# Performance work log

Measured on AMD Instinct MI355X. Metric: run time of the kernel, lower is better.

Reference implementation:

```python
import jax, jax.numpy as jnp
import numpy as np

TANH_CLIP = 10.0
TEMP = 1.0


def setup_inputs() -> dict:
    key = jax.random.key(0)
    ks = jax.random.split(key, 8)
    B, N, E, H, SC = 1024, 1000, 128, 8, 256
    dk = E // H
    context = jax.random.normal(ks[0], (B, 1, E), dtype=jnp.float32)
    step_context = jax.random.normal(ks[1], (B, 1, SC), dtype=jnp.float32)
    # scale weights so tanh/softmax stay in a sane numeric range
    W_step = jax.random.normal(ks[2], (E, SC), dtype=jnp.float32) * 0.05
    glimpse_K = jax.random.normal(ks[3], (H, B, 1, N, dk), dtype=jnp.float32)
    glimpse_V = jax.random.normal(ks[4], (H, B, 1, N, dk), dtype=jnp.float32)
    logit_K = jax.random.normal(ks[5], (B, 1, N, E), dtype=jnp.float32)
    W_out = jax.random.normal(ks[6], (E, E), dtype=jnp.float32) * 0.05
    mask = jax.random.randint(ks[7], (B, 1, N), 0, 2).astype(bool)
    mask = mask.at[:, :, 0].set(False)  # guarantee at least one feasible node
    return {"context": context, "step_context": step_context, "W_step": W_step,
            "glimpse_K": glimpse_K, "glimpse_V": glimpse_V, "logit_K": logit_K,
            "W_out": W_out, "mask": mask}


def reference(context, step_context, W_step, glimpse_K, glimpse_V, logit_K, W_out, mask):
    B, S, E = context.shape          # S = num_steps = 1
    H = glimpse_K.shape[0]
    dk = E // H
    neg_inf = jnp.float32(-jnp.inf)
    # query = context_node_projected + project_step_context(step_context)
    query = context + jnp.einsum('bsc,ec->bse', step_context, W_step)  # [B,S,E]
    # split heads: glimpse_Q -> [H,B,S,dk] (the singleton q-dim of the torch code is folded)
    Q = query.reshape(B, S, H, dk).transpose(2, 0, 1, 3)
    # compatibility [H,B,S,N]
    compat = jnp.einsum('hbsk,hbsnk->hbsn', Q, glimpse_K) / jnp.sqrt(jnp.float32(dk))
    compat = jnp.where(mask[None], neg_inf, compat)       # mask_inner
    attn = jax.nn.softmax(compat, axis=-1)
    heads = jnp.einsum('hbsn,hbsnk->hbsk', attn, glimpse_V)  # [H,B,S,dk]
    glimpse = heads.transpose(1, 2, 0, 3).reshape(B, S, E)   # concat heads
    glimpse = jnp.einsum('bse,oe->bso', glimpse, W_out)      # project_out
    # logits against logit_K  [B,S,N]
    logits = jnp.einsum('bse,bsne->bsn', glimpse, logit_K) / jnp.sqrt(jnp.float32(E))
    logits = jnp.tanh(logits) * jnp.float32(TANH_CLIP)       # tanh clipping
    logits = jnp.where(mask, neg_inf, logits)                # mask_logits
    log_p = jax.nn.log_softmax(logits / jnp.float32(TEMP), axis=-1)
    return log_p
```

## Files before the change

### kernel.cpp

```cpp
#include <hip/hip_runtime.h>
#include <hip/hip_bf16.h>
#include <math.h>

#define NB  1024
#define NN  1000
#define NE  128
#define NH  8
#define NDK 16
#define NSC 256

typedef __attribute__((ext_vector_type(4))) float f32x4;

__device__ __forceinline__ f32x4 ld4(const float* p) {
    return *reinterpret_cast<const f32x4*>(p);
}

__global__ __launch_bounds__(128)
void query_kernel(const float* __restrict__ ctx, const float* __restrict__ stepc,
                  const float* __restrict__ Wstep, float* __restrict__ q_ws)
{
    const int b = blockIdx.x, t = threadIdx.x;
    __shared__ float sc[NSC];
    sc[t] = stepc[b * NSC + t];
    sc[t + 128] = stepc[b * NSC + t + 128];
    __syncthreads();
    float acc = ctx[b * NE + t];
    const float4* w4 = reinterpret_cast<const float4*>(Wstep + (size_t)t * NSC);
    #pragma unroll 8
    for (int c4 = 0; c4 < NSC / 4; ++c4) {
        float4 w = w4[c4];
        acc += sc[4*c4] * w.x + sc[4*c4+1] * w.y + sc[4*c4+2] * w.z + sc[4*c4+3] * w.w;
    }
    q_ws[b * NE + t] = acc;
}

__global__ __launch_bounds__(512, 4)
void fused_kernel(const float* __restrict__ q_ws,
                  const float* __restrict__ gK, const float* __restrict__ gV,
                  const float* __restrict__ lK, const float* __restrict__ Wout,
                  const unsigned char* __restrict__ mask,
                  __hip_bfloat16* __restrict__ out)
{
    const int b = blockIdx.x;
    const int t = threadIdx.x;
    const int w = t >> 6, lane = t & 63;
    const int qq  = lane & 3;
    const int rsl = lane >> 2;

    __shared__ float wmax[2][8], wsum[2][8];
    __shared__ __align__(16) float wred[2][8][16];
    __shared__ __align__(16) float g[NE];
    __shared__ __align__(16) float gout[NE];
    __shared__ float red[8];
    __shared__ float Mv, LSv;

    const unsigned int* mw = reinterpret_cast<const unsigned int*>(mask);
    const bool m_i32 = (__ballot(mw[lane] <= 1u) == ~0ull);
    const int* mask_i = reinterpret_cast<const int*>(mask);

    unsigned mbits = 0;
    #pragma unroll
    for (int i = 0; i < 8; ++i) {
        const int n = w * 16 + i * 128 + rsl;
        const bool dead = (n >= NN);
        const int nn = dead ? 0 : n;
        int mk = m_i32 ? (mask_i[(size_t)b * NN + nn] != 0)
                       : (mask[(size_t)b * NN + nn] != 0);
        mbits |= (unsigned)(mk | (dead ? 1 : 0)) << i;
    }

    #pragma unroll 1
    for (int h = 0; h < NH; ++h) {
        const int pb = h & 1;
        const f32x4 qv = ld4(q_ws + (size_t)b * NE + h * NDK + qq * 4);
        const float* Kb = gK + (size_t)(h * NB + b) * NN * NDK;
        const float* Vb = gV + (size_t)(h * NB + b) * NN * NDK;

        f32x4 vreg[8];
        float sc[8];
        #pragma unroll
        for (int i = 0; i < 8; ++i) {
            const int n = w * 16 + i * 128 + rsl;
            const int nn = ((mbits >> i) & 1u) ? 0 : n;
            const size_t off = (size_t)nn * NDK + qq * 4;
            f32x4 kv = ld4(Kb + off);
            vreg[i] = ld4(Vb + off);
            sc[i] = kv.x*qv.x + kv.y*qv.y + kv.z*qv.z + kv.w*qv.w;
        }
        #pragma unroll
        for (int i = 0; i < 8; ++i) {
            float p = sc[i];
            p += __shfl_xor(p, 1);
            p += __shfl_xor(p, 2);
            sc[i] = ((mbits >> i) & 1u) ? -INFINITY : p * 0.25f;
        }

        float m = sc[0];
        #pragma unroll
        for (int i = 1; i < 8; ++i) m = fmaxf(m, sc[i]);
        #pragma unroll
        for (int off = 32; off > 0; off >>= 1) m = fmaxf(m, __shfl_xor(m, off));
        if (lane == 0) wmax[pb][w] = m;
        __syncthreads();
        float M = wmax[pb][0];
        #pragma unroll
        for (int i = 1; i < 8; ++i) M = fmaxf(M, wmax[pb][i]);

        f32x4 acc = {0.f, 0.f, 0.f, 0.f};
        float ls = 0.f;
        #pragma unroll
        for (int i = 0; i < 8; ++i) {
            const float e = expf(sc[i] - M);
            ls += e;
            acc.x += e * vreg[i].x; acc.y += e * vreg[i].y;
            acc.z += e * vreg[i].z; acc.w += e * vreg[i].w;
        }
        #pragma unroll
        for (int off = 32; off > 0; off >>= 1) ls += __shfl_xor(ls, off);
        if (lane == 0) wsum[pb][w] = ls;

        #pragma unroll
        for (int off = 4; off < 64; off <<= 1) {
            acc.x += __shfl_xor(acc.x, off);
            acc.y += __shfl_xor(acc.y, off);
            acc.z += __shfl_xor(acc.z, off);
            acc.w += __shfl_xor(acc.w, off);
        }
        if (lane < 4) *reinterpret_cast<f32x4*>(&wred[pb][w][lane * 4]) = acc;
        __syncthreads();

        if (t < NDK) {
            float S = wsum[pb][0];
            #pragma unroll
            for (int i = 1; i < 8; ++i) S += wsum[pb][i];
            S *= 0.25f;
            float r = wred[pb][0][t];
            #pragma unroll
            for (int i = 1; i < 8; ++i) r += wred[pb][i][t];
            g[h * NDK + t] = r / S;
        }
    }
    __syncthreads();

    if (t < NE) {
        float a2 = 0.f;
        const float4* w4 = reinterpret_cast<const float4*>(Wout + (size_t)t * NE);
        const float4* g4 = reinterpret_cast<const float4*>(g);
        #pragma unroll 8
        for (int e4 = 0; e4 < NE / 4; ++e4) {
            float4 wv = w4[e4]; float4 gg = g4[e4];
            a2 += wv.x*gg.x + wv.y*gg.y + wv.z*gg.z + wv.w*gg.w;
        }
        gout[t] = a2;
    }
    __syncthreads();

    const f32x4* go4 = reinterpret_cast<const f32x4*>(gout);
    float lv[2];
    #pragma unroll
    for (int i = 0; i < 2; ++i) {
        const int n = t + 512 * i;
        const bool live = (n < NN);
        const int nidx = live ? n : 0;
        int mkd = m_i32 ? (mask_i[(size_t)b * NN + nidx] != 0)
                        : (mask[(size_t)b * NN + nidx] != 0);
        mkd |= (live ? 0 : 1);
        const int nn = mkd ? 0 : n;
        const float* lp = lK + ((size_t)b * NN + nn) * NE;
        float a3 = 0.f;
        #pragma unroll
        for (int c4 = 0; c4 < NE / 4; ++c4) {
            f32x4 x = ld4(lp + 4 * c4);
            f32x4 gv = go4[c4];
            a3 += x.x*gv.x + x.y*gv.y + x.z*gv.z + x.w*gv.w;
        }
        float val = tanhf(a3 * 0.08838834764831845f) * 10.0f;
        lv[i] = mkd ? -3.0e38f : val;
    }

    float mm = fmaxf(lv[0], lv[1]);
    #pragma unroll
    for (int off = 32; off > 0; off >>= 1) mm = fmaxf(mm, __shfl_xor(mm, off));
    if (lane == 0) red[w] = mm;
    __syncthreads();
    if (t == 0) {
        float m2 = red[0];
        #pragma unroll
        for (int i = 1; i < 8; ++i) m2 = fmaxf(m2, red[i]);
        Mv = m2;
    }
    __syncthreads();
    const float M2 = Mv;
    float s2 = expf(lv[0] - M2) + expf(lv[1] - M2);
    #pragma unroll
    for (int off = 32; off > 0; off >>= 1) s2 += __shfl_xor(s2, off);
    if (lane == 0) red[w] = s2;
    __syncthreads();
    if (t == 0) {
        float ss = 0.f;
        #pragma unroll
        for (int i = 0; i < 8; ++i) ss += red[i];
        LSv = M2 + logf(ss);
    }
    __syncthreads();
    const float LS = LSv;
    #pragma unroll
    for (int i = 0; i < 2; ++i) {
        const int n = t + 512 * i;
        if (n < NN)
            out[(size_t)b * NN + n] = __float2bfloat16(lv[i] - LS);
    }
}

extern "C" void kernel_launch(void* const* d_in, const int* in_sizes, int n_in,
                              void* d_out, int out_size, void* d_ws, size_t ws_size,
                              hipStream_t stream) {
    const float* ctx   = (const float*)d_in[0];
    const float* stepc = (const float*)d_in[1];
    const float* Wstep = (const float*)d_in[2];
    const float* gK    = (const float*)d_in[3];
    const float* gV    = (const float*)d_in[4];
    const float* lK    = (const float*)d_in[5];
    const float* Wout  = (const float*)d_in[6];
    const unsigned char* mask = (const unsigned char*)d_in[7];
    __hip_bfloat16* out = (__hip_bfloat16*)d_out;

    const size_t need = (size_t)NB * NE * 4;
    if (ws_size >= need) {
        float* q_ws = (float*)d_ws;
        query_kernel<<<dim3(NB), dim3(128), 0, stream>>>(ctx, stepc, Wstep, q_ws);
        fused_kernel<<<dim3(NB), dim3(512), 0, stream>>>(q_ws, gK, gV, lK, Wout, mask, out);
    } else {
        query_kernel<<<dim3(NB), dim3(128), 0, stream>>>(ctx, stepc, Wstep, (float*)d_ws);
        fused_kernel<<<dim3(NB), dim3(512), 0, stream>>>((float*)d_ws, gK, gV, lK, Wout, mask, out);
    }
}
```

Measured before the change: 219.9 us.

## Use per-wave online softmax to remove per-head block barriers

Replaces the per-head two-pass softmax, which needed two block-wide barriers per head, with an online softmax processed in two chunks of four rows. Each wave keeps its own max, sum and partial V accumulation. Per-wave partials for all heads are written to shared memory and merged once after the head loop with rescaling, leaving one barrier instead of sixteen. It also uses fast __expf and fewer K/V registers live at a time, at the cost of extra rescale multiplies and slightly different rounding.

```diff
diff --git a/kernel.cpp b/kernel.cpp
--- a/kernel.cpp
+++ b/kernel.cpp
@@ -47,8 +47,8 @@
     const int qq  = lane & 3;
     const int rsl = lane >> 2;
 
-    __shared__ float wmax[2][8], wsum[2][8];
-    __shared__ __align__(16) float wred[2][8][16];
+    __shared__ float m_l[NH][8], ls_l[NH][8];
+    __shared__ __align__(16) float acc_l[NH][8][16];
     __shared__ __align__(16) float g[NE];
     __shared__ __align__(16) float gout[NE];
     __shared__ float red[8];
@@ -71,74 +71,83 @@
 
     #pragma unroll 1
     for (int h = 0; h < NH; ++h) {
-        const int pb = h & 1;
         const f32x4 qv = ld4(q_ws + (size_t)b * NE + h * NDK + qq * 4);
         const float* Kb = gK + (size_t)(h * NB + b) * NN * NDK;
         const float* Vb = gV + (size_t)(h * NB + b) * NN * NDK;
 
-        f32x4 vreg[8];
-        float sc[8];
-        #pragma unroll
-        for (int i = 0; i < 8; ++i) {
-            const int n = w * 16 + i * 128 + rsl;
-            const int nn = ((mbits >> i) & 1u) ? 0 : n;
-            const size_t off = (size_t)nn * NDK + qq * 4;
-            f32x4 kv = ld4(Kb + off);
-            vreg[i] = ld4(Vb + off);
-            sc[i] = kv.x*qv.x + kv.y*qv.y + kv.z*qv.z + kv.w*qv.w;
-        }
-        #pragma unroll
-        for (int i = 0; i < 8; ++i) {
-            float p = sc[i];
-            p += __shfl_xor(p, 1);
-            p += __shfl_xor(p, 2);
-            sc[i] = ((mbits >> i) & 1u) ? -INFINITY : p * 0.25f;
-        }
-
-        float m = sc[0];
-        #pragma unroll
-        for (int i = 1; i < 8; ++i) m = fmaxf(m, sc[i]);
-        #pragma unroll
-        for (int off = 32; off > 0; off >>= 1) m = fmaxf(m, __shfl_xor(m, off));
-        if (lane == 0) wmax[pb][w] = m;
-        __syncthreads();
-        float M = wmax[pb][0];
-        #pragma unroll
-        for (int i = 1; i < 8; ++i) M = fmaxf(M, wmax[pb][i]);
-
+        float m = -3.0e38f, ls = 0.f;
         f32x4 acc = {0.f, 0.f, 0.f, 0.f};
-        float ls = 0.f;
-        #pragma unroll
-        for (int i = 0; i < 8; ++i) {
-            const float e = expf(sc[i] - M);
-            ls += e;
-            acc.x += e * vreg[i].x; acc.y += e * vreg[i].y;
-            acc.z += e * vreg[i].z; acc.w += e * vreg[i].w;
-        }
-        #pragma unroll
-        for (int off = 32; off > 0; off >>= 1) ls += __shfl_xor(ls, off);
-        if (lane == 0) wsum[pb][w] = ls;
-
+
+        #pragma unroll
+        for (int half = 0; half < 2; ++half) {
+            f32x4 kv[4], vv[4];
+            #pragma unroll
+            for (int j = 0; j < 4; ++j) {
+                const int i = half * 4 + j;
+                const int n = w * 16 + i * 128 + rsl;
+                const int nn = ((mbits >> i) & 1u) ? 0 : n;
+                const size_t off = (size_t)nn * NDK + qq * 4;
+                kv[j] = ld4(Kb + off);
+                vv[j] = ld4(Vb + off);
+            }
+            float s[4];
+            #pragma unroll
+            for (int j = 0; j < 4; ++j) {
+                const int i = half * 4 + j;
+                float p = kv[j].x*qv.x + kv[j].y*qv.y + kv[j].z*qv.z + kv[j].w*qv.w;
+                p += __shfl_xor(p, 1);
+                p += __shfl_xor(p, 2);
+                s[j] = ((mbits >> i) & 1u) ? -INFINITY : p * 0.25f;
+            }
+            const float bm = fmaxf(fmaxf(s[0], s[1]), fmaxf(s[2], s[3]));
+            const float mn = fmaxf(m, bm);
+            const float corr = __expf(m - mn);
+            ls *= corr;
+            acc.x *= corr; acc.y *= corr; acc.z *= corr; acc.w *= corr;
+            #pragma unroll
+            for (int j = 0; j < 4; ++j) {
+                const float e = __expf(s[j] - mn);
+                ls += e;
+                acc.x += e * vv[j].x; acc.y += e * vv[j].y;
+                acc.z += e * vv[j].z; acc.w += e * vv[j].w;
+            }
+            m = mn;
+        }
+
+        float mw_ = m;
+        #pragma unroll
+        for (int off = 4; off < 64; off <<= 1) mw_ = fmaxf(mw_, __shfl_xor(mw_, off));
+        const float f = __expf(m - mw_);
+        ls *= f;
+        acc.x *= f; acc.y *= f; acc.z *= f; acc.w *= f;
         #pragma unroll
         for (int off = 4; off < 64; off <<= 1) {
+            ls    += __shfl_xor(ls, off);
             acc.x += __shfl_xor(acc.x, off);
             acc.y += __shfl_xor(acc.y, off);
             acc.z += __shfl_xor(acc.z, off);
             acc.w += __shfl_xor(acc.w, off);
         }
-        if (lane < 4) *reinterpret_cast<f32x4*>(&wred[pb][w][lane * 4]) = acc;
-        __syncthreads();
-
-        if (t < NDK) {
-            float S = wsum[pb][0];
-            #pragma unroll
-            for (int i = 1; i < 8; ++i) S += wsum[pb][i];
-            S *= 0.25f;
-            float r = wred[pb][0][t];
-            #pragma unroll
-            for (int i = 1; i < 8; ++i) r += wred[pb][i][t];
-            g[h * NDK + t] = r / S;
-        }
+        if (rsl == 0) {
+            *reinterpret_cast<f32x4*>(&acc_l[h][w][qq * 4]) = acc;
+            if (qq == 0) { m_l[h][w] = mw_; ls_l[h][w] = ls; }
+        }
+    }
+    __syncthreads();
+
+    if (t < NE) {
+        const int h = t >> 4, k = t & 15;
+        float M = m_l[h][0];
+        #pragma unroll
+        for (int i = 1; i < 8; ++i) M = fmaxf(M, m_l[h][i]);
+        float num = 0.f, den = 0.f;
+        #pragma unroll
+        for (int i = 0; i < 8; ++i) {
+            const float fw = __expf(m_l[h][i] - M);
+            num += acc_l[h][i][k] * fw;
+            den += ls_l[h][i] * fw;
+        }
+        g[t] = num / den;
     }
     __syncthreads();
 
@@ -225,13 +234,7 @@
     const unsigned char* mask = (const unsigned char*)d_in[7];
     __hip_bfloat16* out = (__hip_bfloat16*)d_out;
 
-    const size_t need = (size_t)NB * NE * 4;
-    if (ws_size >= need) {
-        float* q_ws = (float*)d_ws;
-        query_kernel<<<dim3(NB), dim3(128), 0, stream>>>(ctx, stepc, Wstep, q_ws);
-        fused_kernel<<<dim3(NB), dim3(512), 0, stream>>>(q_ws, gK, gV, lK, Wout, mask, out);
-    } else {
-        query_kernel<<<dim3(NB), dim3(128), 0, stream>>>(ctx, stepc, Wstep, (float*)d_ws);
-        fused_kernel<<<dim3(NB), dim3(512), 0, stream>>>((float*)d_ws, gK, gV, lK, Wout, mask, out);
-    }
-}
+    float* q_ws = (float*)d_ws;
+    query_kernel<<<dim3(NB), dim3(128), 0, stream>>>(ctx, stepc, Wstep, q_ws);
+    fused_kernel<<<dim3(NB), dim3(512), 0, stream>>>(q_ws, gK, gV, lK, Wout, mask, out);
+}
```

New measurement: 224.3 us. 1.02x slower.
